# Optimization experiments

Hardware: AMD Instinct MI355X
Metric: run time of the kernel (lower is better)

The kernel has to match this reference:

```python
import jax, jax.numpy as jnp
import numpy as np

ENC_DIM, DEC_DIM, JOINT_DIM, VOCAB = 512, 640, 512, 1024
B, T, U = 8, 256, 64


def setup_inputs() -> dict:
    key = jax.random.key(0)
    ks = jax.random.split(key, 8)
    s_enc = 1.0 / np.sqrt(ENC_DIM)
    s_dec = 1.0 / np.sqrt(DEC_DIM)
    s_out = 1.0 / np.sqrt(2 * JOINT_DIM)
    return {
        "enc_out": jax.random.normal(ks[0], (B, T, ENC_DIM), jnp.float32),
        "pred_out": jax.random.normal(ks[1], (B, U, DEC_DIM), jnp.float32),
        "W_enc": jax.random.uniform(ks[2], (JOINT_DIM, ENC_DIM), jnp.float32, -s_enc, s_enc),
        "b_enc": jax.random.uniform(ks[3], (JOINT_DIM,), jnp.float32, -s_enc, s_enc),
        "W_pred": jax.random.uniform(ks[4], (JOINT_DIM, DEC_DIM), jnp.float32, -s_dec, s_dec),
        "b_pred": jax.random.uniform(ks[5], (JOINT_DIM,), jnp.float32, -s_dec, s_dec),
        "W_out": jax.random.uniform(ks[6], (VOCAB, 2 * JOINT_DIM), jnp.float32, -s_out, s_out),
        "b_out": jax.random.uniform(ks[7], (VOCAB,), jnp.float32, -s_out, s_out),
    }


def reference(enc_out, pred_out, W_enc, b_enc, W_pred, b_pred, W_out, b_out):
    # Dropout is identity in eval mode. fc_out on cat([enc_exp, pred_exp]) is
    # mathematically identical to splitting W_out in half and summing two
    # broadcast projections (avoids materializing the [B,T,U,2J] tensor).
    J = W_enc.shape[0]
    e = jnp.einsum('bte,je->btj', enc_out, W_enc) + b_enc    # [B,T,J]
    p = jnp.einsum('bud,jd->buj', pred_out, W_pred) + b_pred  # [B,U,J]
    W1, W2 = W_out[:, :J], W_out[:, J:]
    out = (jnp.einsum('btj,vj->btv', e, W1)[:, :, None, :]
           + jnp.einsum('buj,vj->buv', p, W2)[:, None, :, :]
           + b_out)                                           # [B,T,U,V]
    return out
```

## Files before the change

### kernel.cpp

```cpp
#include <hip/hip_runtime.h>

typedef float f4 __attribute__((ext_vector_type(4)));
typedef float f32x4 __attribute__((ext_vector_type(4)));
typedef short bf16x8 __attribute__((ext_vector_type(8)));
typedef unsigned short u16x8 __attribute__((ext_vector_type(8)));

static __device__ __forceinline__ unsigned short f2bf(float f) {
    unsigned int x = __builtin_bit_cast(unsigned int, f);
    x = (x + 0x7fffu + ((x >> 16) & 1u)) >> 16;
    return (unsigned short)x;
}
static __device__ __forceinline__ float bf2f(unsigned short h) {
    unsigned int x = ((unsigned int)h) << 16;
    return __builtin_bit_cast(float, x);
}

static __device__ __forceinline__ void gll16(const unsigned short* g, unsigned short* l) {
    __builtin_amdgcn_global_load_lds(
        (__attribute__((address_space(1))) void*)(g),
        (__attribute__((address_space(3))) void*)(l), 16, 0, 0);
}

struct CvtJob { const float* src; unsigned short* hi; unsigned short* lo; int n8; };

__global__ __launch_bounds__(256) void convert_kernel(
    CvtJob j0, CvtJob j1, CvtJob j2, CvtJob j3, CvtJob j4, int total8)
{
    CvtJob jobs[5] = { j0, j1, j2, j3, j4 };
    int cum1 = j0.n8, cum2 = cum1 + j1.n8, cum3 = cum2 + j2.n8, cum4 = cum3 + j3.n8;
    for (int g = blockIdx.x * blockDim.x + threadIdx.x; g < total8;
         g += gridDim.x * blockDim.x) {
        int ji, base;
        if      (g < cum1) { ji = 0; base = 0; }
        else if (g < cum2) { ji = 1; base = cum1; }
        else if (g < cum3) { ji = 2; base = cum2; }
        else if (g < cum4) { ji = 3; base = cum3; }
        else               { ji = 4; base = cum4; }
        const CvtJob& J = jobs[ji];
        int idx = (g - base) * 8;
        f4 a = *(const f4*)(J.src + idx);
        f4 b = *(const f4*)(J.src + idx + 4);
        u16x8 hv, lv;
        float s[8] = { a.x, a.y, a.z, a.w, b.x, b.y, b.z, b.w };
        #pragma unroll
        for (int i = 0; i < 8; ++i) {
            unsigned short h = f2bf(s[i]);
            hv[i] = h;
            lv[i] = f2bf(s[i] - bf2f(h));
        }
        *(u16x8*)(J.hi + idx) = hv;
        *(u16x8*)(J.lo + idx) = lv;
    }
}

struct GJob {
    const unsigned short *Ah, *Al, *Wh, *Wl;
    int lda, ldw;
    const float* bias;
    float* Cf;
    unsigned short *Ch, *Cl;
    int N, K, nbx;
};

static __device__ __forceinline__ int fragoff(int r, int s) {
    return r * 32 + ((s ^ ((r >> 1) & 3)) << 3);
}

template<bool SPLIT_OUT>
__global__ __launch_bounds__(256, 3) void gemm64(GJob j0, GJob j1, int nblk0)
{
    __shared__ unsigned short lds[2][4][64 * 32];

    const bool first = (int)blockIdx.x < nblk0;
    const GJob J = first ? j0 : j1;
    const int local = first ? (int)blockIdx.x : (int)blockIdx.x - nblk0;
    const int m0 = (local % J.nbx) * 64;
    const int n0 = (local / J.nbx) * 64;

    const int tid  = threadIdx.x;
    const int lane = tid & 63;
    const int wid  = tid >> 6;
    const int wr   = wid >> 1, wc = wid & 1;
    const int lrow = lane & 15;
    const int s    = lane >> 4;

    const int srow  = wid * 16 + (lane >> 2);
    const int sslot = (lane & 3) ^ ((srow >> 1) & 3);
    const size_t gA = (size_t)(m0 + srow) * J.lda + sslot * 8;
    const size_t gW = (size_t)(n0 + srow) * J.ldw + sslot * 8;

    f32x4 acc[2][2];
    #pragma unroll
    for (int i = 0; i < 2; ++i)
        #pragma unroll
        for (int j = 0; j < 2; ++j) acc[i][j] = (f32x4){0.f, 0.f, 0.f, 0.f};

    const int nt = J.K / 32;

    gll16(J.Ah + gA, &lds[0][0][wid * 512]);
    gll16(J.Al + gA, &lds[0][1][wid * 512]);
    gll16(J.Wh + gW, &lds[0][2][wid * 512]);
    gll16(J.Wl + gW, &lds[0][3][wid * 512]);
    asm volatile("s_waitcnt vmcnt(0)" ::: "memory");
    __syncthreads();

    int cur = 0;
    for (int t = 0; t < nt; ++t) {
        if (t + 1 < nt) {
            const int k0 = (t + 1) * 32;
            gll16(J.Ah + gA + k0, &lds[cur ^ 1][0][wid * 512]);
            gll16(J.Al + gA + k0, &lds[cur ^ 1][1][wid * 512]);
            gll16(J.Wh + gW + k0, &lds[cur ^ 1][2][wid * 512]);
            gll16(J.Wl + gW + k0, &lds[cur ^ 1][3][wid * 512]);
        }

        bf16x8 ah[2], al[2], wh[2], wl[2];
        #pragma unroll
        for (int i = 0; i < 2; ++i) {
            const int ra = wr * 32 + i * 16 + lrow;
            const int rw = wc * 32 + i * 16 + lrow;
            ah[i] = *(const bf16x8*)&lds[cur][0][fragoff(ra, s)];
            al[i] = *(const bf16x8*)&lds[cur][1][fragoff(ra, s)];
            wh[i] = *(const bf16x8*)&lds[cur][2][fragoff(rw, s)];
            wl[i] = *(const bf16x8*)&lds[cur][3][fragoff(rw, s)];
        }
        #pragma unroll
        for (int i = 0; i < 2; ++i)
            #pragma unroll
            for (int j = 0; j < 2; ++j) {
                acc[i][j] = __builtin_amdgcn_mfma_f32_16x16x32_bf16(ah[i], wh[j], acc[i][j], 0, 0, 0);
                acc[i][j] = __builtin_amdgcn_mfma_f32_16x16x32_bf16(ah[i], wl[j], acc[i][j], 0, 0, 0);
                acc[i][j] = __builtin_amdgcn_mfma_f32_16x16x32_bf16(al[i], wh[j], acc[i][j], 0, 0, 0);
            }

        if (t + 1 < nt) {
            asm volatile("s_waitcnt vmcnt(0)" ::: "memory");
            __syncthreads();
            cur ^= 1;
        }
    }

    #pragma unroll
    for (int i = 0; i < 2; ++i) {
        const int rbase = m0 + wr * 32 + i * 16 + (lane >> 4) * 4;
        #pragma unroll
        for (int j = 0; j < 2; ++j) {
            const int col = n0 + wc * 32 + j * 16 + (lane & 15);
            const float bv = J.bias ? J.bias[col] : 0.f;
            #pragma unroll
            for (int r = 0; r < 4; ++r) {
                float v = acc[i][j][r] + bv;
                size_t off = (size_t)(rbase + r) * J.N + col;
                if (SPLIT_OUT) {
                    unsigned short h = f2bf(v);
                    J.Ch[off] = h;
                    J.Cl[off] = f2bf(v - bf2f(h));
                } else {
                    J.Cf[off] = v;
                }
            }
        }
    }
}

__global__ __launch_bounds__(256) void bcast_kernel(
    const float* __restrict__ X, const float* __restrict__ Y,
    float* __restrict__ out, int T, int U)
{
    const int Vq  = 256;
    const int bt  = blockIdx.x;
    const int b   = bt / T;
    const int tid = threadIdx.x;

    const f4* X4 = (const f4*)X;
    const f4* Y4 = (const f4*)Y + (size_t)b * U * Vq;
    f4* O4 = (f4*)out + (size_t)bt * U * Vq;

    f4 x = X4[(size_t)bt * Vq + tid];
    #pragma unroll 4
    for (int u = 0; u < U; ++u) {
        f4 y = Y4[u * Vq + tid];
        f4 r = { x.x + y.x, x.y + y.y, x.z + y.z, x.w + y.w };
        __builtin_nontemporal_store(r, &O4[u * Vq + tid]);
    }
}

extern "C" void kernel_launch(void* const* d_in, const int* in_sizes, int n_in,
                              void* d_out, int out_size, void* d_ws, size_t ws_size,
                              hipStream_t stream) {
    (void)in_sizes; (void)n_in; (void)out_size; (void)ws_size;

    const int B = 8, T = 256, U = 64;
    const int ENC = 512, DEC = 640, J = 512, V = 1024;
    const int MT = B * T;
    const int MU = B * U;

    const float* enc    = (const float*)d_in[0];
    const float* pred   = (const float*)d_in[1];
    const float* W_enc  = (const float*)d_in[2];
    const float* b_enc  = (const float*)d_in[3];
    const float* W_pred = (const float*)d_in[4];
    const float* b_pred = (const float*)d_in[5];
    const float* W_out  = (const float*)d_in[6];
    const float* b_out  = (const float*)d_in[7];
    float* out = (float*)d_out;

    const int n_enc  = MT * ENC;
    const int n_pred = MU * DEC;
    const int n_We   = J * ENC;
    const int n_Wp   = J * DEC;
    const int n_Wo   = V * 2 * J;
    const int n_e    = MT * J;
    const int n_p    = MU * J;

    unsigned short* w = (unsigned short*)d_ws;
    unsigned short* enc_h  = w;
    unsigned short* enc_l  = enc_h + n_enc;
    unsigned short* pred_h = enc_l + n_enc;
    unsigned short* pred_l = pred_h + n_pred;
    unsigned short* We_h   = pred_l + n_pred;
    unsigned short* We_l   = We_h + n_We;
    unsigned short* Wp_h   = We_l + n_We;
    unsigned short* Wp_l   = Wp_h + n_Wp;
    unsigned short* Wo_h   = Wp_l + n_Wp;
    unsigned short* Wo_l   = Wo_h + n_Wo;
    unsigned short* e_h    = Wo_l + n_Wo;
    unsigned short* e_l    = e_h + n_e;
    unsigned short* p_h    = e_l + n_e;
    unsigned short* p_l    = p_h + n_p;
    float* ws_X = (float*)(p_l + n_p);
    float* ws_Y = ws_X + (size_t)MT * V;

    CvtJob j0 = { enc,    enc_h,  enc_l,  n_enc  / 8 };
    CvtJob j1 = { pred,   pred_h, pred_l, n_pred / 8 };
    CvtJob j2 = { W_enc,  We_h,   We_l,   n_We   / 8 };
    CvtJob j3 = { W_pred, Wp_h,   Wp_l,   n_Wp   / 8 };
    CvtJob j4 = { W_out,  Wo_h,   Wo_l,   n_Wo   / 8 };
    const int total8 = (n_enc + n_pred + n_We + n_Wp + n_Wo) / 8;
    convert_kernel<<<(total8 + 255) / 256, 256, 0, stream>>>(j0, j1, j2, j3, j4, total8);

    GJob je = { enc_h, enc_l, We_h, We_l, ENC, ENC, b_enc,
                nullptr, e_h, e_l, J, ENC, MT / 64 };
    GJob jp = { pred_h, pred_l, Wp_h, Wp_l, DEC, DEC, b_pred,
                nullptr, p_h, p_l, J, DEC, MU / 64 };
    const int nbe = (MT / 64) * (J / 64);
    const int nbp = (MU / 64) * (J / 64);
    gemm64<true><<<nbe + nbp, 256, 0, stream>>>(je, jp, nbe);

    GJob jx = { e_h, e_l, Wo_h, Wo_l, J, 2 * J, b_out,
                ws_X, nullptr, nullptr, V, J, MT / 64 };
    GJob jy = { p_h, p_l, Wo_h + J, Wo_l + J, J, 2 * J, nullptr,
                ws_Y, nullptr, nullptr, V, J, MU / 64 };
    const int nbx = (MT / 64) * (V / 64);
    const int nby = (MU / 64) * (V / 64);
    gemm64<false><<<nbx + nby, 256, 0, stream>>>(jx, jy, nbx);

    bcast_kernel<<<dim3(B * T), 256, 0, stream>>>(ws_X, ws_Y, out, T, U);
}
```

Baseline: 145.1 us.

## Enlarge GEMM tiles to 128x128 and add grouped block-index remapping

```diff
diff --git a/kernel.cpp b/kernel.cpp
--- a/kernel.cpp
+++ b/kernel.cpp
@@ -67,15 +67,18 @@
 }
 
 template<bool SPLIT_OUT>
-__global__ __launch_bounds__(256, 3) void gemm64(GJob j0, GJob j1, int nblk0)
+__global__ __launch_bounds__(256, 2) void gemm128(GJob j0, GJob j1, int nblk0)
 {
-    __shared__ unsigned short lds[2][4][64 * 32];
+    __shared__ unsigned short lds[2][4][128 * 32];
 
     const bool first = (int)blockIdx.x < nblk0;
     const GJob J = first ? j0 : j1;
-    const int local = first ? (int)blockIdx.x : (int)blockIdx.x - nblk0;
-    const int m0 = (local % J.nbx) * 64;
-    const int n0 = (local / J.nbx) * 64;
+    const int raw  = first ? (int)blockIdx.x : (int)blockIdx.x - nblk0;
+    const int nblk = first ? nblk0 : ((int)gridDim.x - nblk0);
+    const int q = nblk >> 3;
+    const int local = (raw & 7) * q + (raw >> 3);
+    const int m0 = (local % J.nbx) * 128;
+    const int n0 = (local / J.nbx) * 128;
 
     const int tid  = threadIdx.x;
     const int lane = tid & 63;
@@ -84,50 +87,59 @@
     const int lrow = lane & 15;
     const int s    = lane >> 4;
 
-    const int srow  = wid * 16 + (lane >> 2);
-    const int sslot = (lane & 3) ^ ((srow >> 1) & 3);
-    const size_t gA = (size_t)(m0 + srow) * J.lda + sslot * 8;
-    const size_t gW = (size_t)(n0 + srow) * J.ldw + sslot * 8;
-
-    f32x4 acc[2][2];
+    const int rr = lane >> 2;
+    const int g0 = wid * 32 + rr;
+    const int g1 = g0 + 16;
+    const int sl0 = (lane & 3) ^ ((g0 >> 1) & 3);
+    const int sl1 = (lane & 3) ^ ((g1 >> 1) & 3);
+    const size_t gA0 = (size_t)(m0 + g0) * J.lda + sl0 * 8;
+    const size_t gA1 = (size_t)(m0 + g1) * J.lda + sl1 * 8;
+    const size_t gW0 = (size_t)(n0 + g0) * J.ldw + sl0 * 8;
+    const size_t gW1 = (size_t)(n0 + g1) * J.ldw + sl1 * 8;
+    const int l0 = (wid * 32) * 32;
+    const int l1 = l0 + 16 * 32;
+
+#define STAGE(buf, k0) do { \
+    gll16(J.Ah + gA0 + (k0), &lds[buf][0][l0]); \
+    gll16(J.Ah + gA1 + (k0), &lds[buf][0][l1]); \
+    gll16(J.Al + gA0 + (k0), &lds[buf][1][l0]); \
+    gll16(J.Al + gA1 + (k0), &lds[buf][1][l1]); \
+    gll16(J.Wh + gW0 + (k0), &lds[buf][2][l0]); \
+    gll16(J.Wh + gW1 + (k0), &lds[buf][2][l1]); \
+    gll16(J.Wl + gW0 + (k0), &lds[buf][3][l0]); \
+    gll16(J.Wl + gW1 + (k0), &lds[buf][3][l1]); \
+} while (0)
+
+    f32x4 acc[4][4];
     #pragma unroll
-    for (int i = 0; i < 2; ++i)
-        #pragma unroll
-        for (int j = 0; j < 2; ++j) acc[i][j] = (f32x4){0.f, 0.f, 0.f, 0.f};
+    for (int i = 0; i < 4; ++i)
+        #pragma unroll
+        for (int j = 0; j < 4; ++j) acc[i][j] = (f32x4){0.f, 0.f, 0.f, 0.f};
 
     const int nt = J.K / 32;
 
-    gll16(J.Ah + gA, &lds[0][0][wid * 512]);
-    gll16(J.Al + gA, &lds[0][1][wid * 512]);
-    gll16(J.Wh + gW, &lds[0][2][wid * 512]);
-    gll16(J.Wl + gW, &lds[0][3][wid * 512]);
+    STAGE(0, 0);
     asm volatile("s_waitcnt vmcnt(0)" ::: "memory");
     __syncthreads();
 
     int cur = 0;
     for (int t = 0; t < nt; ++t) {
-        if (t + 1 < nt) {
-            const int k0 = (t + 1) * 32;
-            gll16(J.Ah + gA + k0, &lds[cur ^ 1][0][wid * 512]);
-            gll16(J.Al + gA + k0, &lds[cur ^ 1][1][wid * 512]);
-            gll16(J.Wh + gW + k0, &lds[cur ^ 1][2][wid * 512]);
-            gll16(J.Wl + gW + k0, &lds[cur ^ 1][3][wid * 512]);
-        }
-
-        bf16x8 ah[2], al[2], wh[2], wl[2];
-        #pragma unroll
-        for (int i = 0; i < 2; ++i) {
-            const int ra = wr * 32 + i * 16 + lrow;
-            const int rw = wc * 32 + i * 16 + lrow;
+        if (t + 1 < nt) STAGE(cur ^ 1, (t + 1) * 32);
+
+        bf16x8 ah[4], al[4], wh[4], wl[4];
+        #pragma unroll
+        for (int i = 0; i < 4; ++i) {
+            const int ra = wr * 64 + i * 16 + lrow;
+            const int rw = wc * 64 + i * 16 + lrow;
             ah[i] = *(const bf16x8*)&lds[cur][0][fragoff(ra, s)];
             al[i] = *(const bf16x8*)&lds[cur][1][fragoff(ra, s)];
             wh[i] = *(const bf16x8*)&lds[cur][2][fragoff(rw, s)];
             wl[i] = *(const bf16x8*)&lds[cur][3][fragoff(rw, s)];
         }
         #pragma unroll
-        for (int i = 0; i < 2; ++i)
+        for (int i = 0; i < 4; ++i)
             #pragma unroll
-            for (int j = 0; j < 2; ++j) {
+            for (int j = 0; j < 4; ++j) {
                 acc[i][j] = __builtin_amdgcn_mfma_f32_16x16x32_bf16(ah[i], wh[j], acc[i][j], 0, 0, 0);
                 acc[i][j] = __builtin_amdgcn_mfma_f32_16x16x32_bf16(ah[i], wl[j], acc[i][j], 0, 0, 0);
                 acc[i][j] = __builtin_amdgcn_mfma_f32_16x16x32_bf16(al[i], wh[j], acc[i][j], 0, 0, 0);
@@ -139,13 +151,14 @@
             cur ^= 1;
         }
     }
+#undef STAGE
 
     #pragma unroll
-    for (int i = 0; i < 2; ++i) {
-        const int rbase = m0 + wr * 32 + i * 16 + (lane >> 4) * 4;
-        #pragma unroll
-        for (int j = 0; j < 2; ++j) {
-            const int col = n0 + wc * 32 + j * 16 + (lane & 15);
+    for (int i = 0; i < 4; ++i) {
+        const int rbase = m0 + wr * 64 + i * 16 + (lane >> 4) * 4;
+        #pragma unroll
+        for (int j = 0; j < 4; ++j) {
+            const int col = n0 + wc * 64 + j * 16 + (lane & 15);
             const float bv = J.bias ? J.bias[col] : 0.f;
             #pragma unroll
             for (int r = 0; r < 4; ++r) {
@@ -240,20 +253,20 @@
     convert_kernel<<<(total8 + 255) / 256, 256, 0, stream>>>(j0, j1, j2, j3, j4, total8);
 
     GJob je = { enc_h, enc_l, We_h, We_l, ENC, ENC, b_enc,
-                nullptr, e_h, e_l, J, ENC, MT / 64 };
+                nullptr, e_h, e_l, J, ENC, MT / 128 };
     GJob jp = { pred_h, pred_l, Wp_h, Wp_l, DEC, DEC, b_pred,
-                nullptr, p_h, p_l, J, DEC, MU / 64 };
-    const int nbe = (MT / 64) * (J / 64);
-    const int nbp = (MU / 64) * (J / 64);
-    gemm64<true><<<nbe + nbp, 256, 0, stream>>>(je, jp, nbe);
+                nullptr, p_h, p_l, J, DEC, MU / 128 };
+    const int nbe = (MT / 128) * (J / 128);
+    const int nbp = (MU / 128) * (J / 128);
+    gemm128<true><<<nbe + nbp, 256, 0, stream>>>(je, jp, nbe);
 
     GJob jx = { e_h, e_l, Wo_h, Wo_l, J, 2 * J, b_out,
-                ws_X, nullptr, nullptr, V, J, MT / 64 };
+                ws_X, nullptr, nullptr, V, J, MT / 128 };
     GJob jy = { p_h, p_l, Wo_h + J, Wo_l + J, J, 2 * J, nullptr,
-                ws_Y, nullptr, nullptr, V, J, MU / 64 };
-    const int nbx = (MT / 64) * (V / 64);
-    const int nby = (MU / 64) * (V / 64);
-    gemm64<false><<<nbx + nby, 256, 0, stream>>>(jx, jy, nbx);
+                ws_Y, nullptr, nullptr, V, J, MU / 128 };
+    const int nbx = (MT / 128) * (V / 128);
+    const int nby = (MU / 128) * (V / 128);
+    gemm128<false><<<nbx + nby, 256, 0, stream>>>(jx, jy, nbx);
 
     bcast_kernel<<<dim3(B * T), 256, 0, stream>>>(ws_X, ws_Y, out, T, U);
 }
```

Result: slower. 159.0 us (+9.5%).

## Fuse fp32-to-split-bf16 conversion into first GEMM and drop convert kernel

Applied to the files above, without the earlier changes.

```diff
diff --git a/kernel.cpp b/kernel.cpp
--- a/kernel.cpp
+++ b/kernel.cpp
@@ -21,35 +21,149 @@
         (__attribute__((address_space(3))) void*)(l), 16, 0, 0);
 }
 
-struct CvtJob { const float* src; unsigned short* hi; unsigned short* lo; int n8; };
-
-__global__ __launch_bounds__(256) void convert_kernel(
-    CvtJob j0, CvtJob j1, CvtJob j2, CvtJob j3, CvtJob j4, int total8)
+static __device__ __forceinline__ int fragoff(int r, int s) {
+    return r * 32 + ((s ^ ((r >> 1) & 3)) << 3);
+}
+
+struct GJobF {
+    const float *A, *W;
+    int lda, ldw;
+    const float* bias;
+    unsigned short *Ch, *Cl;
+    int N, K, nbx;
+};
+
+__global__ __launch_bounds__(256, 3) void gemmcvt64(
+    GJobF j0, GJobF j1, int nblk0, int nblk1,
+    const float* __restrict__ Wo, unsigned short* __restrict__ Wo_h,
+    unsigned short* __restrict__ Wo_l, int nWo8)
 {
-    CvtJob jobs[5] = { j0, j1, j2, j3, j4 };
-    int cum1 = j0.n8, cum2 = cum1 + j1.n8, cum3 = cum2 + j2.n8, cum4 = cum3 + j3.n8;
-    for (int g = blockIdx.x * blockDim.x + threadIdx.x; g < total8;
-         g += gridDim.x * blockDim.x) {
-        int ji, base;
-        if      (g < cum1) { ji = 0; base = 0; }
-        else if (g < cum2) { ji = 1; base = cum1; }
-        else if (g < cum3) { ji = 2; base = cum2; }
-        else if (g < cum4) { ji = 3; base = cum3; }
-        else               { ji = 4; base = cum4; }
-        const CvtJob& J = jobs[ji];
-        int idx = (g - base) * 8;
-        f4 a = *(const f4*)(J.src + idx);
-        f4 b = *(const f4*)(J.src + idx + 4);
-        u16x8 hv, lv;
-        float s[8] = { a.x, a.y, a.z, a.w, b.x, b.y, b.z, b.w };
-        #pragma unroll
-        for (int i = 0; i < 8; ++i) {
-            unsigned short h = f2bf(s[i]);
-            hv[i] = h;
-            lv[i] = f2bf(s[i] - bf2f(h));
-        }
-        *(u16x8*)(J.hi + idx) = hv;
-        *(u16x8*)(J.lo + idx) = lv;
+    __shared__ unsigned short lds[2][4][64 * 32];
+
+    const int bid = blockIdx.x;
+    const int tid = threadIdx.x;
+
+    if (bid >= nblk0 + nblk1) {
+        const int nblkc = (int)gridDim.x - nblk0 - nblk1;
+        for (int g = (bid - nblk0 - nblk1) * 256 + tid; g < nWo8; g += nblkc * 256) {
+            const int idx = g * 8;
+            f4 a = *(const f4*)(Wo + idx);
+            f4 b = *(const f4*)(Wo + idx + 4);
+            u16x8 hv, lv;
+            float s[8] = { a.x, a.y, a.z, a.w, b.x, b.y, b.z, b.w };
+            #pragma unroll
+            for (int i = 0; i < 8; ++i) {
+                unsigned short h = f2bf(s[i]);
+                hv[i] = h;
+                lv[i] = f2bf(s[i] - bf2f(h));
+            }
+            *(u16x8*)(Wo_h + idx) = hv;
+            *(u16x8*)(Wo_l + idx) = lv;
+        }
+        return;
+    }
+
+    const bool first = bid < nblk0;
+    const GJobF J = first ? j0 : j1;
+    const int local = first ? bid : bid - nblk0;
+    const int m0 = (local % J.nbx) * 64;
+    const int n0 = (local / J.nbx) * 64;
+
+    const int lane = tid & 63;
+    const int wid  = tid >> 6;
+    const int wr   = wid >> 1, wc = wid & 1;
+    const int lrow = lane & 15;
+    const int s    = lane >> 4;
+
+    const int row  = tid >> 2, slot = tid & 3;
+    const int woff = fragoff(row, slot);
+    const float* pA = J.A + (size_t)(m0 + row) * J.lda + slot * 8;
+    const float* pW = J.W + (size_t)(n0 + row) * J.ldw + slot * 8;
+
+    f4 ra0, ra1, rw0, rw1;
+
+#define LOADREGS(k0) do { \
+    ra0 = *(const f4*)(pA + (k0));     ra1 = *(const f4*)(pA + (k0) + 4); \
+    rw0 = *(const f4*)(pW + (k0));     rw1 = *(const f4*)(pW + (k0) + 4); \
+} while (0)
+
+#define CVTWRITE(buf) do { \
+    u16x8 ha, la, hw, lw; \
+    float sa[8] = { ra0.x, ra0.y, ra0.z, ra0.w, ra1.x, ra1.y, ra1.z, ra1.w }; \
+    float sw[8] = { rw0.x, rw0.y, rw0.z, rw0.w, rw1.x, rw1.y, rw1.z, rw1.w }; \
+    _Pragma("unroll") \
+    for (int i = 0; i < 8; ++i) { \
+        unsigned short h = f2bf(sa[i]); \
+        ha[i] = h; la[i] = f2bf(sa[i] - bf2f(h)); \
+        h = f2bf(sw[i]); \
+        hw[i] = h; lw[i] = f2bf(sw[i] - bf2f(h)); \
+    } \
+    *(u16x8*)&lds[buf][0][woff] = ha; \
+    *(u16x8*)&lds[buf][1][woff] = la; \
+    *(u16x8*)&lds[buf][2][woff] = hw; \
+    *(u16x8*)&lds[buf][3][woff] = lw; \
+} while (0)
+
+    f32x4 acc[2][2];
+    #pragma unroll
+    for (int i = 0; i < 2; ++i)
+        #pragma unroll
+        for (int j = 0; j < 2; ++j) acc[i][j] = (f32x4){0.f, 0.f, 0.f, 0.f};
+
+    const int nt = J.K / 32;
+
+    LOADREGS(0);
+    CVTWRITE(0);
+    __syncthreads();
+
+    int cur = 0;
+    for (int t = 0; t < nt; ++t) {
+        if (t + 1 < nt) LOADREGS((t + 1) * 32);
+
+        bf16x8 ah[2], al[2], wh[2], wl[2];
+        #pragma unroll
+        for (int i = 0; i < 2; ++i) {
+            const int ra = wr * 32 + i * 16 + lrow;
+            const int rw = wc * 32 + i * 16 + lrow;
+            ah[i] = *(const bf16x8*)&lds[cur][0][fragoff(ra, s)];
+            al[i] = *(const bf16x8*)&lds[cur][1][fragoff(ra, s)];
+            wh[i] = *(const bf16x8*)&lds[cur][2][fragoff(rw, s)];
+            wl[i] = *(const bf16x8*)&lds[cur][3][fragoff(rw, s)];
+        }
+        #pragma unroll
+        for (int i = 0; i < 2; ++i)
+            #pragma unroll
+            for (int j = 0; j < 2; ++j) {
+                acc[i][j] = __builtin_amdgcn_mfma_f32_16x16x32_bf16(ah[i], wh[j], acc[i][j], 0, 0, 0);
+                acc[i][j] = __builtin_amdgcn_mfma_f32_16x16x32_bf16(ah[i], wl[j], acc[i][j], 0, 0, 0);
+                acc[i][j] = __builtin_amdgcn_mfma_f32_16x16x32_bf16(al[i], wh[j], acc[i][j], 0, 0, 0);
+            }
+
+        if (t + 1 < nt) {
+            CVTWRITE(cur ^ 1);
+            __syncthreads();
+            cur ^= 1;
+        }
+    }
+#undef LOADREGS
+#undef CVTWRITE
+
+    #pragma unroll
+    for (int i = 0; i < 2; ++i) {
+        const int rbase = m0 + wr * 32 + i * 16 + (lane >> 4) * 4;
+        #pragma unroll
+        for (int j = 0; j < 2; ++j) {
+            const int col = n0 + wc * 32 + j * 16 + (lane & 15);
+            const float bv = J.bias[col];
+            #pragma unroll
+            for (int r = 0; r < 4; ++r) {
+                float v = acc[i][j][r] + bv;
+                size_t off = (size_t)(rbase + r) * J.N + col;
+                unsigned short h = f2bf(v);
+                J.Ch[off] = h;
+                J.Cl[off] = f2bf(v - bf2f(h));
+            }
+        }
     }
 }
 
@@ -58,15 +172,9 @@
     int lda, ldw;
     const float* bias;
     float* Cf;
-    unsigned short *Ch, *Cl;
     int N, K, nbx;
 };
 
-static __device__ __forceinline__ int fragoff(int r, int s) {
-    return r * 32 + ((s ^ ((r >> 1) & 3)) << 3);
-}
-
-template<bool SPLIT_OUT>
 __global__ __launch_bounds__(256, 3) void gemm64(GJob j0, GJob j1, int nblk0)
 {
     __shared__ unsigned short lds[2][4][64 * 32];
@@ -148,17 +256,8 @@
             const int col = n0 + wc * 32 + j * 16 + (lane & 15);
             const float bv = J.bias ? J.bias[col] : 0.f;
             #pragma unroll
-            for (int r = 0; r < 4; ++r) {
-                float v = acc[i][j][r] + bv;
-                size_t off = (size_t)(rbase + r) * J.N + col;
-                if (SPLIT_OUT) {
-                    unsigned short h = f2bf(v);
-                    J.Ch[off] = h;
-                    J.Cl[off] = f2bf(v - bf2f(h));
-                } else {
-                    J.Cf[off] = v;
-                }
-            }
+            for (int r = 0; r < 4; ++r)
+                J.Cf[(size_t)(rbase + r) * J.N + col] = acc[i][j][r] + bv;
         }
     }
 }
@@ -205,55 +304,33 @@
     const float* b_out  = (const float*)d_in[7];
     float* out = (float*)d_out;
 
-    const int n_enc  = MT * ENC;
-    const int n_pred = MU * DEC;
-    const int n_We   = J * ENC;
-    const int n_Wp   = J * DEC;
-    const int n_Wo   = V * 2 * J;
-    const int n_e    = MT * J;
-    const int n_p    = MU * J;
+    const int n_Wo = V * 2 * J;
+    const int n_e  = MT * J;
+    const int n_p  = MU * J;
 
     unsigned short* w = (unsigned short*)d_ws;
-    unsigned short* enc_h  = w;
-    unsigned short* enc_l  = enc_h + n_enc;
-    unsigned short* pred_h = enc_l + n_enc;
-    unsigned short* pred_l = pred_h + n_pred;
-    unsigned short* We_h   = pred_l + n_pred;
-    unsigned short* We_l   = We_h + n_We;
-    unsigned short* Wp_h   = We_l + n_We;
-    unsigned short* Wp_l   = Wp_h + n_Wp;
-    unsigned short* Wo_h   = Wp_l + n_Wp;
-    unsigned short* Wo_l   = Wo_h + n_Wo;
-    unsigned short* e_h    = Wo_l + n_Wo;
-    unsigned short* e_l    = e_h + n_e;
-    unsigned short* p_h    = e_l + n_e;
-    unsigned short* p_l    = p_h + n_p;
+    unsigned short* Wo_h = w;
+    unsigned short* Wo_l = Wo_h + n_Wo;
+    unsigned short* e_h  = Wo_l + n_Wo;
+    unsigned short* e_l  = e_h + n_e;
+    unsigned short* p_h  = e_l + n_e;
+    unsigned short* p_l  = p_h + n_p;
     float* ws_X = (float*)(p_l + n_p);
     float* ws_Y = ws_X + (size_t)MT * V;
 
-    CvtJob j0 = { enc,    enc_h,  enc_l,  n_enc  / 8 };
-    CvtJob j1 = { pred,   pred_h, pred_l, n_pred / 8 };
-    CvtJob j2 = { W_enc,  We_h,   We_l,   n_We   / 8 };
-    CvtJob j3 = { W_pred, Wp_h,   Wp_l,   n_Wp   / 8 };
-    CvtJob j4 = { W_out,  Wo_h,   Wo_l,   n_Wo   / 8 };
-    const int total8 = (n_enc + n_pred + n_We + n_Wp + n_Wo) / 8;
-    convert_kernel<<<(total8 + 255) / 256, 256, 0, stream>>>(j0, j1, j2, j3, j4, total8);
-
-    GJob je = { enc_h, enc_l, We_h, We_l, ENC, ENC, b_enc,
-                nullptr, e_h, e_l, J, ENC, MT / 64 };
-    GJob jp = { pred_h, pred_l, Wp_h, Wp_l, DEC, DEC, b_pred,
-                nullptr, p_h, p_l, J, DEC, MU / 64 };
+    GJobF je = { enc,  W_enc,  ENC, ENC, b_enc,  e_h, e_l, J, ENC, MT / 64 };
+    GJobF jp = { pred, W_pred, DEC, DEC, b_pred, p_h, p_l, J, DEC, MU / 64 };
     const int nbe = (MT / 64) * (J / 64);
     const int nbp = (MU / 64) * (J / 64);
-    gemm64<true><<<nbe + nbp, 256, 0, stream>>>(je, jp, nbe);
-
-    GJob jx = { e_h, e_l, Wo_h, Wo_l, J, 2 * J, b_out,
-                ws_X, nullptr, nullptr, V, J, MT / 64 };
-    GJob jy = { p_h, p_l, Wo_h + J, Wo_l + J, J, 2 * J, nullptr,
-                ws_Y, nullptr, nullptr, V, J, MU / 64 };
+    const int ncv = 64;
+    gemmcvt64<<<nbe + nbp + ncv, 256, 0, stream>>>(
+        je, jp, nbe, nbp, W_out, Wo_h, Wo_l, n_Wo / 8);
+
+    GJob jx = { e_h, e_l, Wo_h, Wo_l, J, 2 * J, b_out, ws_X, V, J, MT / 64 };
+    GJob jy = { p_h, p_l, Wo_h + J, Wo_l + J, J, 2 * J, nullptr, ws_Y, V, J, MU / 64 };
     const int nbx = (MT / 64) * (V / 64);
     const int nby = (MU / 64) * (V / 64);
-    gemm64<false><<<nbx + nby, 256, 0, stream>>>(jx, jy, nbx);
+    gemm64<<<nbx + nby, 256, 0, stream>>>(jx, jy, nbx);
 
     bcast_kernel<<<dim3(B * T), 256, 0, stream>>>(ws_X, ws_Y, out, T, U);
 }
```

After: 136.3 us. -6.1%, faster.
